# Optimization experiments

Measured on AMD Instinct MI355X. Metric: run time of the kernel, lower is better.

## Reference

```python
import jax, jax.numpy as jnp
import numpy as np
from jax import lax

N_RAYS, N_STEPS, G = 4096, 160, 160
COLOR_DIM, WIDTH = 3, 128
POS_PE, VIEW_PE = 5, 4
XYZ_MIN, XYZ_MAX = -1.0, 1.0
NEAR = 0.05
STEPSIZE = 0.5
VOXEL_SIZE = (XYZ_MAX - XYZ_MIN) / G
DIST = STEPSIZE * VOXEL_SIZE
S_VAL = 80.0
FASTCOLOR_THRES = 1e-7
MASK_THRES = 1e-3
ALPHA_INIT = 1e-4
ACT_SHIFT = float(np.log(1.0 / (1.0 - ALPHA_INIT) - 1.0))
SMOOTH_K, SMOOTH_SIGMA = 5, 1.0
POSFREQ = jnp.asarray([2.0 ** i for i in range(POS_PE)], jnp.float32)
VIEWFREQ = jnp.asarray([2.0 ** i for i in range(VIEW_PE)], jnp.float32)


def _gauss_kernel():
    ax = np.arange(SMOOTH_K) - SMOOTH_K // 2
    g = np.exp(-(ax ** 2) / (2.0 * SMOOTH_SIGMA ** 2))
    k = g[:, None, None] * g[None, :, None] * g[None, None, :]
    return jnp.asarray(k / k.sum(), np.float32)[None, None]


def _trilerp(grid, pts):
    # grid [C,Gx,Gx,Gx]; pts [...,3] in world coords -> [..., C] (align_corners trilinear)
    Gx = grid.shape[-1]
    u = (pts - XYZ_MIN) / (XYZ_MAX - XYZ_MIN) * (Gx - 1)
    u = jnp.clip(u, 0.0, Gx - 1.0)
    i0 = jnp.clip(jnp.floor(u).astype(jnp.int32), 0, Gx - 2)
    f = u - i0.astype(u.dtype)
    x0, y0, z0 = i0[..., 0], i0[..., 1], i0[..., 2]
    fx, fy, fz = f[..., 0], f[..., 1], f[..., 2]
    def g8(ix, iy, iz):
        return grid[:, ix, iy, iz]  # [C, ...]
    out = (g8(x0, y0, z0) * (1 - fx) * (1 - fy) * (1 - fz)
         + g8(x0, y0, z0 + 1) * (1 - fx) * (1 - fy) * fz
         + g8(x0, y0 + 1, z0) * (1 - fx) * fy * (1 - fz)
         + g8(x0, y0 + 1, z0 + 1) * (1 - fx) * fy * fz
         + g8(x0 + 1, y0, z0) * fx * (1 - fy) * (1 - fz)
         + g8(x0 + 1, y0, z0 + 1) * fx * (1 - fy) * fz
         + g8(x0 + 1, y0 + 1, z0) * fx * fy * (1 - fz)
         + g8(x0 + 1, y0 + 1, z0 + 1) * fx * fy * fz)
    return jnp.moveaxis(out, 0, -1)


def _alphas2weights(alpha):
    # per-ray (segmented) exclusive cumprod of transmittance; alpha [N,S]
    T = jnp.cumprod(1.0 - alpha, axis=1)
    T_excl = jnp.concatenate([jnp.ones_like(T[:, :1]), T[:, :-1]], axis=1)
    return alpha * T_excl, T[:, -1]


def _mlp(x, w0, b0, w1, b1, w2, b2):
    h = jax.nn.relu(x @ w0 + b0)
    h = jax.nn.relu(h @ w1 + b1)
    return h @ w2 + b2


def _forward(rays_o, rays_d, viewdirs, sdf_grid, mask_density,
             off_color_grid, emo_color_grid,
             off_w0, off_b0, off_w1, off_b1, off_w2, off_b2,
             emo_w0, emo_b0, emo_w1, emo_b1, emo_w2, emo_b2, em_modes):
    N = rays_o.shape[0]
    t = NEAR + DIST * jnp.arange(N_STEPS, dtype=jnp.float32)
    ray_pts = rays_o[:, None, :] + rays_d[:, None, :] * t[None, :, None]  # [N,S,3]

    # MaskCache: threshold alpha from coarse density grid (boolean keep mask)
    dens = _trilerp(mask_density, ray_pts)[..., 0]
    mask_alpha = 1.0 - jnp.exp(-jax.nn.softplus(dens + ACT_SHIFT) * DIST)
    keep0 = mask_alpha >= MASK_THRES  # [N,S]

    # Gaussian-smoothed SDF grid + central-difference gradient grid
    sdf_s = lax.conv_general_dilated(sdf_grid, _gauss_kernel(), (1, 1, 1), 'SAME',
                                     dimension_numbers=('NCDHW', 'OIDHW', 'NCDHW'))[0]  # [1,G,G,G]
    s = sdf_s[0]
    grad_grid = jnp.zeros((3, G, G, G), sdf_grid.dtype)
    grad_grid = grad_grid.at[0, 1:-1].set((s[2:] - s[:-2]) / (2 * VOXEL_SIZE))
    grad_grid = grad_grid.at[1, :, 1:-1].set((s[:, 2:] - s[:, :-2]) / (2 * VOXEL_SIZE))
    grad_grid = grad_grid.at[2, :, :, 1:-1].set((s[:, :, 2:] - s[:, :, :-2]) / (2 * VOXEL_SIZE))

    sdf = _trilerp(sdf_s, ray_pts)[..., 0]   # [N,S]
    gradient = _trilerp(grad_grid, ray_pts)  # [N,S,3]

    # NeuS alpha from sdf (scatter, grad variant, cos_anneal = 1)
    true_cos = jnp.einsum('nd,nsd->ns', viewdirs, gradient)
    iter_cos = -jax.nn.relu(-true_cos)
    prev_cdf = jax.nn.sigmoid((sdf - iter_cos * DIST * 0.5) * S_VAL)
    next_cdf = jax.nn.sigmoid((sdf + iter_cos * DIST * 0.5) * S_VAL)
    alpha = jnp.clip((prev_cdf - next_cdf + 1e-5) / (prev_cdf + 1e-5), 0.0, 1.0)
    alpha = jnp.where(keep0, alpha, 0.0)  # masked points contribute nothing

    weights, _ = _alphas2weights(alpha)
    keep1 = weights > FASTCOLOR_THRES
    alpha = jnp.where(keep1, alpha, 0.0)
    weights, alphainv_last = _alphas2weights(alpha)

    # features: pos PE, view PE (per-ray, gathered by ray_id == broadcast), normal
    rays_xyz = (ray_pts - XYZ_MIN) / (XYZ_MAX - XYZ_MIN)  # [N,S,3]
    xyz_emb = (rays_xyz[..., None] * POSFREQ).reshape(N, N_STEPS, -1)
    v_emb = (viewdirs[..., None] * VIEWFREQ).reshape(N, -1)
    v_full = jnp.concatenate([v_emb, jnp.sin(v_emb), jnp.cos(v_emb)], -1)
    v_full = jnp.broadcast_to(v_full[:, None, :], (N, N_STEPS, v_full.shape[-1]))
    normal = gradient / (jnp.linalg.norm(gradient, axis=-1, keepdims=True) + 1e-5)
    rgb_feat = jnp.concatenate([rays_xyz, jnp.sin(xyz_emb), jnp.cos(xyz_emb), v_full, normal], -1)

    off_in = jnp.concatenate([_trilerp(off_color_grid, ray_pts), rgb_feat], -1)
    emo_in = jnp.concatenate([_trilerp(emo_color_grid, ray_pts), rgb_feat], -1)
    off_rgb = jax.nn.sigmoid(_mlp(off_in, off_w0, off_b0, off_w1, off_b1, off_w2, off_b2))
    emo_rgb = jax.nn.sigmoid(_mlp(emo_in, emo_w0, emo_b0, emo_w1, emo_b1, emo_w2, emo_b2))
    on_mask = (em_modes == 1)[:, None, None]  # em_modes[ray_id] == 1
    rgb = jnp.where(on_mask, emo_rgb, 0.0) + off_rgb

    w_ = weights[..., None]
    rgb_marched = jnp.sum(w_ * rgb, axis=1)  # segment_coo(sum over ray_id)
    cum_weights = jnp.sum(w_, axis=1)        # [N,1]
    return rgb_marched, alphainv_last, 1.0 - cum_weights


def setup_inputs() -> dict:
    key = jax.random.key(0)
    ks = jax.random.split(key, 12)
    rays_o = jax.random.uniform(ks[0], (N_RAYS, 3), jnp.float32, -0.3, 0.3)
    rd = jax.random.normal(ks[1], (N_RAYS, 3), jnp.float32)
    rays_d = rd / jnp.linalg.norm(rd, axis=-1, keepdims=True)
    viewdirs = rays_d
    em_modes = jax.random.randint(ks[2], (N_RAYS,), 0, 2)
    lin = np.linspace(-1.0, 1.0, G, dtype=np.float32)
    x, y, z = np.meshgrid(lin, lin, lin, indexing='ij')
    sdf_grid = jnp.asarray(np.sqrt(x ** 2 + y ** 2 + z ** 2) - 1.0)[None, None]  # sphere-SDF init
    mask_density = jax.random.normal(ks[3], (1, 80, 80, 80), jnp.float32) * 2.0 + 12.0
    off_color_grid = jax.random.normal(ks[4], (COLOR_DIM, G, G, G), jnp.float32) * 0.1
    emo_color_grid = jax.random.normal(ks[5], (COLOR_DIM, G, G, G), jnp.float32) * 0.1
    DIM0 = 3 + 3 * POS_PE * 2 + 3 * VIEW_PE * 3 + COLOR_DIM + 3  # = 75
    def lw(k, i, o):
        return jax.random.normal(k, (i, o), jnp.float32) * (1.0 / np.sqrt(i))
    return dict(rays_o=rays_o, rays_d=rays_d, viewdirs=viewdirs, em_modes=em_modes,
                sdf_grid=sdf_grid, mask_density=mask_density,
                off_color_grid=off_color_grid, emo_color_grid=emo_color_grid,
                off_w0=lw(ks[6], DIM0, WIDTH), off_b0=jnp.zeros((WIDTH,), jnp.float32),
                off_w1=lw(ks[7], WIDTH, WIDTH), off_b1=jnp.zeros((WIDTH,), jnp.float32),
                off_w2=lw(ks[8], WIDTH, 3), off_b2=jnp.zeros((3,), jnp.float32),
                emo_w0=lw(ks[9], DIM0, WIDTH), emo_b0=jnp.zeros((WIDTH,), jnp.float32),
                emo_w1=lw(ks[10], WIDTH, WIDTH), emo_b1=jnp.zeros((WIDTH,), jnp.float32),
                emo_w2=lw(ks[11], WIDTH, 3), emo_b2=jnp.zeros((3,), jnp.float32))


def reference(rays_o, rays_d, viewdirs, em_modes, sdf_grid, mask_density,
              off_color_grid, emo_color_grid,
              off_w0, off_b0, off_w1, off_b1, off_w2, off_b2,
              emo_w0, emo_b0, emo_w1, emo_b1, emo_w2, emo_b2):
    return _forward(rays_o, rays_d, viewdirs, sdf_grid, mask_density,
                    off_color_grid, emo_color_grid,
                    off_w0, off_b0, off_w1, off_b1, off_w2, off_b2,
                    emo_w0, emo_b0, emo_w1, emo_b1, emo_w2, emo_b2, em_modes)
```

## Files before the change

kernel.cpp:

```cpp
#include <hip/hip_runtime.h>

#define NRAYS 4096
#define NSTEPS 160
#define NSAMP (NRAYS*NSTEPS)
#define GG 160
#define GG2 (GG*GG)
#define GG3 (GG*GG2)
#define GM 80
#define GM2 (GM*GM)

#define NEARV 0.05f
#define DISTV 0.00625f
#define SVAL 80.0f
#define ACT_SHIFT_C (-9.2102403669758813f)
#define INV2H 40.0f
#define MASK_THRES_C 1e-3f
#define FAST_THRES_C 1e-7f

#define KW0 0.05448868454964295f
#define KW1 0.24420134200323332f
#define KW2 0.40261994689424750f

__device__ __forceinline__ float sigmf(float x){ return 1.0f/(1.0f+__expf(-x)); }
__device__ __forceinline__ float softplusf_(float x){ return (x>20.0f)? x : log1pf(__expf(x)); }

__device__ __forceinline__ void tricoord(float p, int Gx, int& i0, float& fr){
  float u = (p + 1.0f)*0.5f*(float)(Gx-1);
  u = fminf(fmaxf(u, 0.0f), (float)(Gx-1));
  int i = (int)floorf(u);
  i = min(max(i,0), Gx-2);
  i0 = i; fr = u - (float)i;
}

__global__ __launch_bounds__(256) void ksmooth_yz(const float* __restrict__ in, float* __restrict__ out,
                                                  float* __restrict__ outbuf, int* __restrict__ cnt){
  __shared__ float S[36][37];
  __shared__ float Tz[36][33];
  const int bx = blockIdx.x;
  const int t = threadIdx.x;
  if (bx == 0){
    for (int i = t; i < NRAYS*3; i += 256) outbuf[i] = 0.0f;
    if (t == 0) *cnt = 0;
  }
  const int x  = bx / 25;
  const int tile = bx % 25;
  const int Y0 = (tile/5)*32, Z0 = (tile%5)*32;
  const float kw[5] = {KW0,KW1,KW2,KW1,KW0};
  for (int i = t; i < 36*36; i += 256){
    int r = i/36, c = i - (i/36)*36;
    int y = Y0 + r - 2, z = Z0 + c - 2;
    float v = 0.0f;
    if (y>=0 && y<GG && z>=0 && z<GG) v = in[(x*GG+y)*GG+z];
    S[r][c] = v;
  }
  __syncthreads();
  for (int i = t; i < 36*32; i += 256){
    int r = i >> 5, c = i & 31;
    float acc = 0.f;
    #pragma unroll
    for (int d=0; d<5; d++) acc += kw[d]*S[r][c+d];
    Tz[r][c] = acc;
  }
  __syncthreads();
  for (int i = t; i < 32*32; i += 256){
    int yy = i >> 5, c = i & 31;
    float acc = 0.f;
    #pragma unroll
    for (int d=0; d<5; d++) acc += kw[d]*Tz[yy+d][c];
    out[(x*GG + Y0+yy)*GG + Z0 + c] = acc;
  }
}

__global__ __launch_bounds__(64) void kmarch(
  const float* __restrict__ ro, const float* __restrict__ rd,
  const float* __restrict__ vd, const float* __restrict__ maskg,
  const float* __restrict__ Y,
  int* __restrict__ slist, float* __restrict__ sw, float* __restrict__ sgrad,
  int* __restrict__ cnt, float* __restrict__ out)
{
  int n = blockIdx.x*64 + threadIdx.x;
  if (n >= NRAYS) return;
  const float ox=ro[n*3+0], oy=ro[n*3+1], oz=ro[n*3+2];
  const float dx=rd[n*3+0], dy=rd[n*3+1], dz=rd[n*3+2];
  const float vx=vd[n*3+0], vy=vd[n*3+1], vz=vd[n*3+2];
  const float kwc[5] = {KW0,KW1,KW2,KW1,KW0};
  float T1=1.0f, T2=1.0f, cum=0.0f;
  for (int s=0; s<NSTEPS; s++){
    float tt = NEARV + DISTV*(float)s;
    float px = ox + dx*tt, py = oy + dy*tt, pz = oz + dz*tt;

    int mx,my,mz; float mfx,mfy,mfz;
    tricoord(px, GM, mx, mfx); tricoord(py, GM, my, mfy); tricoord(pz, GM, mz, mfz);
    int mid = (mx*GM + my)*GM + mz;
    float d000=maskg[mid],        d001=maskg[mid+1];
    float d010=maskg[mid+GM],     d011=maskg[mid+GM+1];
    float d100=maskg[mid+GM2],    d101=maskg[mid+GM2+1];
    float d110=maskg[mid+GM2+GM], d111=maskg[mid+GM2+GM+1];
    float m00 = d000 + (d001-d000)*mfz;
    float m01 = d010 + (d011-d010)*mfz;
    float m10 = d100 + (d101-d100)*mfz;
    float m11 = d110 + (d111-d110)*mfz;
    float m0 = m00 + (m01-m00)*mfy;
    float m1 = m10 + (m11-m10)*mfy;
    float dens = m0 + (m1-m0)*mfx;
    float malpha = 1.0f - __expf(-softplusf_(dens + ACT_SHIFT_C)*DISTV);

    int ix,iy,iz; float fx,fy,fz;
    tricoord(px, GG, ix, fx); tricoord(py, GG, iy, fy); tricoord(pz, GG, iz, fz);

    float R[2][2][8];
    #pragma unroll
    for (int jb=0;jb<2;jb++)
      #pragma unroll
      for (int jc=0;jc<2;jc++)
        #pragma unroll
        for (int j=0;j<8;j++){
          int a = ix-3+j;
          R[jb][jc][j] = (a>=0 && a<GG) ? Y[(a*GG + iy+jb)*GG + iz+jc] : 0.0f;
        }
    const bool hasym = (iy>=1), hasyp = (iy<=GG-3);
    const bool haszm = (iz>=1), haszp = (iz<=GG-3);
    float Eym[2][6], Eyp[2][6], Ezm[2][6], Ezp[2][6];
    #pragma unroll
    for (int jc=0;jc<2;jc++)
      #pragma unroll
      for (int j=0;j<6;j++){
        int a = ix-2+j;
        bool ax = (a>=0 && a<GG);
        Eym[jc][j] = (hasym && ax) ? Y[(a*GG + iy-1)*GG + iz+jc] : 0.0f;
        Eyp[jc][j] = (hasyp && ax) ? Y[(a*GG + iy+2)*GG + iz+jc] : 0.0f;
      }
    #pragma unroll
    for (int jb=0;jb<2;jb++)
      #pragma unroll
      for (int j=0;j<6;j++){
        int a = ix-2+j;
        bool ax = (a>=0 && a<GG);
        Ezm[jb][j] = (haszm && ax) ? Y[(a*GG + iy+jb)*GG + iz-1] : 0.0f;
        Ezp[jb][j] = (haszp && ax) ? Y[(a*GG + iy+jb)*GG + iz+2] : 0.0f;
      }

    float sdf=0.0f, gx=0.0f, gy=0.0f, gz=0.0f;
    #pragma unroll
    for (int ja=0;ja<2;ja++){
      #pragma unroll
      for (int jb=0;jb<2;jb++){
        #pragma unroll
        for (int jc=0;jc<2;jc++){
          float w = (ja?fx:1.0f-fx)*(jb?fy:1.0f-fy)*(jc?fz:1.0f-fz);
          const float* r = R[jb][jc];
          float s0=0.0f;
          #pragma unroll
          for (int t2=0;t2<5;t2++) s0 += kwc[t2]*r[ja+1+t2];
          sdf += w*s0;
          int a = ix+ja, b = iy+jb, c = iz+jc;
          if (a>=1 && a<=GG-2){
            float sp=0.0f, sm=0.0f;
            #pragma unroll
            for (int t2=0;t2<5;t2++){ sp += kwc[t2]*r[ja+2+t2]; sm += kwc[t2]*r[ja+t2]; }
            gx += w*INV2H*(sp-sm);
          }
          if (b>=1 && b<=GG-2){
            float acc=0.0f;
            if (jb==0){
              const float* up = R[1][jc];
              const float* dn = Eym[jc];
              #pragma unroll
              for (int t2=0;t2<5;t2++) acc += kwc[t2]*(up[ja+1+t2] - dn[ja+t2]);
            } else {
              const float* up = Eyp[jc];
              const float* dn = R[0][jc];
              #pragma unroll
              for (int t2=0;t2<5;t2++) acc += kwc[t2]*(up[ja+t2] - dn[ja+1+t2]);
            }
            gy += w*INV2H*acc;
          }
          if (c>=1 && c<=GG-2){
            float acc=0.0f;
            if (jc==0){
              const float* up = R[jb][1];
              const float* dn = Ezm[jb];
              #pragma unroll
              for (int t2=0;t2<5;t2++) acc += kwc[t2]*(up[ja+1+t2] - dn[ja+t2]);
            } else {
              const float* up = Ezp[jb];
              const float* dn = R[jb][0];
              #pragma unroll
              for (int t2=0;t2<5;t2++) acc += kwc[t2]*(up[ja+t2] - dn[ja+1+t2]);
            }
            gz += w*INV2H*acc;
          }
        }
      }
    }

    float tc = vx*gx + vy*gy + vz*gz;
    float icos = fminf(tc, 0.0f);
    float e = icos*DISTV*0.5f;
    float prev = sigmf((sdf - e)*SVAL);
    float nxt  = sigmf((sdf + e)*SVAL);
    float alpha = (prev - nxt + 1e-5f)/(prev + 1e-5f);
    alpha = fminf(fmaxf(alpha, 0.0f), 1.0f);
    if (!(malpha >= MASK_THRES_C)) alpha = 0.0f;

    float w1 = alpha*T1; T1 *= (1.0f - alpha);
    float a2 = (w1 > FAST_THRES_C) ? alpha : 0.0f;
    float wv = a2*T2;   T2 *= (1.0f - a2);
    cum += wv;
    if (wv > 0.0f){
      int pos = atomicAdd(cnt, 1);
      slist[pos] = n*NSTEPS + s;
      sw[pos] = wv;
      sgrad[pos*3+0]=gx; sgrad[pos*3+1]=gy; sgrad[pos*3+2]=gz;
    }
    if (T1 <= FAST_THRES_C) break;
  }
  out[NRAYS*3 + n] = T2;
  out[NRAYS*4 + n] = 1.0f - cum;
}

__global__ __launch_bounds__(256) void kmlp3(
  const float* __restrict__ ro, const float* __restrict__ rd,
  const float* __restrict__ vd, const int* __restrict__ em,
  const float* __restrict__ offc, const float* __restrict__ emoc,
  const int* __restrict__ slist, const float* __restrict__ sw,
  const float* __restrict__ sgrad, const int* __restrict__ cnt,
  const float* __restrict__ W0o, const float* __restrict__ b0o,
  const float* __restrict__ W1o, const float* __restrict__ b1o,
  const float* __restrict__ W2o, const float* __restrict__ b2o,
  const float* __restrict__ W0e, const float* __restrict__ b0e,
  const float* __restrict__ W1e, const float* __restrict__ b1e,
  const float* __restrict__ W2e, const float* __restrict__ b2e,
  float* __restrict__ out)
{
  __shared__ float X[8][80];
  __shared__ float H[8][132];
  __shared__ float H2[8][132];
  __shared__ float OUTB[8][3];
  __shared__ float WSH[8];
  __shared__ float GS[8][3];
  __shared__ int SSAMP[8];
  __shared__ int SEM[8];
  __shared__ int s_go;

  const int t = threadIdx.x;
  const int count = *cnt;
  const int head = blockIdx.x & 1;
  const int cstride = gridDim.x >> 1;

  const float* W0 = head ? W0e : W0o;  const float* b0 = head ? b0e : b0o;
  const float* W1 = head ? W1e : W1o;  const float* b1 = head ? b1e : b1o;
  const float* W2 = head ? W2e : W2o;  const float* b2 = head ? b2e : b2o;
  const float* cg = head ? emoc : offc;
  const float4* W04 = (const float4*)W0;
  const float4* W14 = (const float4*)W1;

  const int sp   = t >> 5;
  const int lane = t & 31;

  for (int chunk = blockIdx.x >> 1; chunk*8 < count; chunk += cstride) {
    const int base = chunk*8;
    if (t == 0) s_go = 0;
    if (t < 8) {
      int i = base + t;
      bool vld = (i < count);
      int samp = vld ? slist[i] : 0;
      SSAMP[t] = samp;
      WSH[t]   = vld ? sw[i] : 0.0f;
      GS[t][0] = vld ? sgrad[i*3+0] : 0.0f;
      GS[t][1] = vld ? sgrad[i*3+1] : 0.0f;
      GS[t][2] = vld ? sgrad[i*3+2] : 0.0f;
      SEM[t]   = vld ? em[samp/NSTEPS] : 0;
    }
    __syncthreads();
    if (t < 8) {
      bool live = (WSH[t] > 0.0f) && (head == 0 || SEM[t] != 0);
      if (live) s_go = 1;
    }
    __syncthreads();

    if (s_go) {
      {
        const int s = t & 7;
        const int r = t >> 3;
        const int samp = SSAMP[s];
        const int n = samp / NSTEPS;
        const int step = samp - n*NSTEPS;
        const float tt = NEARV + DISTV*(float)step;
        const float px = ro[n*3+0] + rd[n*3+0]*tt;
        const float py = ro[n*3+1] + rd[n*3+1]*tt;
        const float pz = ro[n*3+2] + rd[n*3+2]*tt;
        if (r < 3) {
          int ix,iy,iz; float fx,fy,fz;
          tricoord(px, GG, ix, fx); tricoord(py, GG, iy, fy); tricoord(pz, GG, iz, fz);
          const float* g = cg + (size_t)r * GG3;
          const int id = (ix*GG + iy)*GG + iz;
          float v000=g[id],        v001=g[id+1];
          float v010=g[id+GG],     v011=g[id+GG+1];
          float v100=g[id+GG2],    v101=g[id+GG2+1];
          float v110=g[id+GG2+GG], v111=g[id+GG2+GG+1];
          float c00 = v000 + (v001-v000)*fz;
          float c01 = v010 + (v011-v010)*fz;
          float c10 = v100 + (v101-v100)*fz;
          float c11 = v110 + (v111-v110)*fz;
          float c0 = c00 + (c01-c00)*fy;
          float c1 = c10 + (c11-c10)*fy;
          X[s][r] = c0 + (c1-c0)*fx;
        } else if (r == 3) {
          X[s][3] = (px+1.0f)*0.5f;
          X[s][4] = (py+1.0f)*0.5f;
          X[s][5] = (pz+1.0f)*0.5f;
          float gx = GS[s][0], gy = GS[s][1], gz = GS[s][2];
          float inv = 1.0f/(sqrtf(gx*gx+gy*gy+gz*gz)+1e-5f);
          X[s][72] = gx*inv; X[s][73] = gy*inv; X[s][74] = gz*inv;
        } else if (r < 7) {
          const int a = r - 4;
          const float coord = (a==0)?px:((a==1)?py:pz);
          const float rxyz = (coord+1.0f)*0.5f;
          float fr = 1.0f;
          #pragma unroll
          for (int q = 0; q < 5; q++) {
            float e = rxyz*fr; fr *= 2.0f;
            X[s][6  + a*5 + q] = __sinf(e);
            X[s][21 + a*5 + q] = __cosf(e);
          }
        } else if (r < 10) {
          const int a = r - 7;
          const float v = vd[n*3+a];
          float fr = 1.0f;
          #pragma unroll
          for (int q = 0; q < 4; q++) {
            float e = v*fr; fr *= 2.0f;
            X[s][36 + a*4 + q] = e;
            X[s][48 + a*4 + q] = __sinf(e);
            X[s][60 + a*4 + q] = __cosf(e);
          }
        }
      }
      __syncthreads();

      {
        float4 acc = ((const float4*)b0)[lane];
        #pragma unroll 5
        for (int k=0; k<75; k++){
          float x = X[sp][k];
          float4 w = W04[k*32 + lane];
          acc.x += x*w.x; acc.y += x*w.y; acc.z += x*w.z; acc.w += x*w.w;
        }
        H[sp][lane*4+0] = fmaxf(acc.x,0.0f);
        H[sp][lane*4+1] = fmaxf(acc.y,0.0f);
        H[sp][lane*4+2] = fmaxf(acc.z,0.0f);
        H[sp][lane*4+3] = fmaxf(acc.w,0.0f);
      }
      __syncthreads();

      {
        float4 acc = ((const float4*)b1)[lane];
        #pragma unroll 8
        for (int k=0; k<128; k++){
          float x = H[sp][k];
          float4 w = W14[k*32 + lane];
          acc.x += x*w.x; acc.y += x*w.y; acc.z += x*w.z; acc.w += x*w.w;
        }
        H2[sp][lane*4+0] = fmaxf(acc.x,0.0f);
        H2[sp][lane*4+1] = fmaxf(acc.y,0.0f);
        H2[sp][lane*4+2] = fmaxf(acc.z,0.0f);
        H2[sp][lane*4+3] = fmaxf(acc.w,0.0f);
      }
      __syncthreads();

      {
        float a0=0.0f, a1=0.0f, a2v=0.0f;
        #pragma unroll
        for (int i=0;i<4;i++){
          int k = lane*4+i;
          float h = H2[sp][k];
          a0  += h*W2[k*3+0];
          a1  += h*W2[k*3+1];
          a2v += h*W2[k*3+2];
        }
        #pragma unroll
        for (int d=16; d>=1; d>>=1){
          a0  += __shfl_down(a0,  d, 32);
          a1  += __shfl_down(a1,  d, 32);
          a2v += __shfl_down(a2v, d, 32);
        }
        if (lane == 0){
          OUTB[sp][0] = sigmf(a0  + b2[0]);
          OUTB[sp][1] = sigmf(a1  + b2[1]);
          OUTB[sp][2] = sigmf(a2v + b2[2]);
        }
      }
      __syncthreads();

      if (t < 24) {
        int s2 = t/3, c = t - s2*3;
        float w = WSH[s2];
        if (w > 0.0f && (head == 0 || SEM[s2] != 0)) {
          int n2 = SSAMP[s2]/NSTEPS;
          atomicAdd(&out[n2*3 + c], w * OUTB[s2][c]);
        }
      }
    }
    __syncthreads();
  }
}

extern "C" void kernel_launch(void* const* d_in, const int* in_sizes, int n_in,
                              void* d_out, int out_size, void* d_ws, size_t ws_size,
                              hipStream_t stream) {
  const float* ro    = (const float*)d_in[0];
  const float* rd    = (const float*)d_in[1];
  const float* vd    = (const float*)d_in[2];
  const int*   em    = (const int*)d_in[3];
  const float* sdfg  = (const float*)d_in[4];
  const float* maskg = (const float*)d_in[5];
  const float* offc  = (const float*)d_in[6];
  const float* emoc  = (const float*)d_in[7];
  const float* W0o = (const float*)d_in[8];
  const float* b0o = (const float*)d_in[9];
  const float* W1o = (const float*)d_in[10];
  const float* b1o = (const float*)d_in[11];
  const float* W2o = (const float*)d_in[12];
  const float* b2o = (const float*)d_in[13];
  const float* W0e = (const float*)d_in[14];
  const float* b0e = (const float*)d_in[15];
  const float* W1e = (const float*)d_in[16];
  const float* b1e = (const float*)d_in[17];
  const float* W2e = (const float*)d_in[18];
  const float* b2e = (const float*)d_in[19];

  float* out = (float*)d_out;
  float* ws  = (float*)d_ws;
  float* bufB  = ws;
  float* swb   = ws + GG3;
  float* sgradb= swb + NSAMP;
  int*   slist = (int*)(sgradb + 3*(size_t)NSAMP);
  int*   cnt   = slist + NSAMP;

  ksmooth_yz<<<GG*25, 256, 0, stream>>>(sdfg, bufB, out, cnt);

  kmarch<<<NRAYS/64, 64, 0, stream>>>(ro, rd, vd, maskg, bufB,
                                      slist, swb, sgradb, cnt, out);

  kmlp3<<<2048, 256, 0, stream>>>(ro, rd, vd, em, offc, emoc,
                                  slist, swb, sgradb, cnt,
                                  W0o,b0o,W1o,b1o,W2o,b2o,
                                  W0e,b0e,W1e,b1e,W2e,b2e, out);
}
```

Baseline: 66.89 us.

## Fuse smoothing, ray march and MLP into one cooperative kernel

```diff
diff --git a/kernel.cpp b/kernel.cpp
--- a/kernel.cpp
+++ b/kernel.cpp
@@ -1,4 +1,6 @@
 #include <hip/hip_runtime.h>
+#include <hip/hip_cooperative_groups.h>
+namespace cg = cooperative_groups;
 
 #define NRAYS 4096
 #define NSTEPS 160
@@ -32,207 +34,22 @@
   i0 = i; fr = u - (float)i;
 }
 
-__global__ __launch_bounds__(256) void ksmooth_yz(const float* __restrict__ in, float* __restrict__ out,
-                                                  float* __restrict__ outbuf, int* __restrict__ cnt){
-  __shared__ float S[36][37];
-  __shared__ float Tz[36][33];
-  const int bx = blockIdx.x;
-  const int t = threadIdx.x;
-  if (bx == 0){
-    for (int i = t; i < NRAYS*3; i += 256) outbuf[i] = 0.0f;
-    if (t == 0) *cnt = 0;
-  }
-  const int x  = bx / 25;
-  const int tile = bx % 25;
-  const int Y0 = (tile/5)*32, Z0 = (tile%5)*32;
-  const float kw[5] = {KW0,KW1,KW2,KW1,KW0};
-  for (int i = t; i < 36*36; i += 256){
-    int r = i/36, c = i - (i/36)*36;
-    int y = Y0 + r - 2, z = Z0 + c - 2;
-    float v = 0.0f;
-    if (y>=0 && y<GG && z>=0 && z<GG) v = in[(x*GG+y)*GG+z];
-    S[r][c] = v;
-  }
-  __syncthreads();
-  for (int i = t; i < 36*32; i += 256){
-    int r = i >> 5, c = i & 31;
-    float acc = 0.f;
-    #pragma unroll
-    for (int d=0; d<5; d++) acc += kw[d]*S[r][c+d];
-    Tz[r][c] = acc;
-  }
-  __syncthreads();
-  for (int i = t; i < 32*32; i += 256){
-    int yy = i >> 5, c = i & 31;
-    float acc = 0.f;
-    #pragma unroll
-    for (int d=0; d<5; d++) acc += kw[d]*Tz[yy+d][c];
-    out[(x*GG + Y0+yy)*GG + Z0 + c] = acc;
-  }
-}
-
-__global__ __launch_bounds__(64) void kmarch(
-  const float* __restrict__ ro, const float* __restrict__ rd,
-  const float* __restrict__ vd, const float* __restrict__ maskg,
-  const float* __restrict__ Y,
-  int* __restrict__ slist, float* __restrict__ sw, float* __restrict__ sgrad,
-  int* __restrict__ cnt, float* __restrict__ out)
-{
-  int n = blockIdx.x*64 + threadIdx.x;
-  if (n >= NRAYS) return;
-  const float ox=ro[n*3+0], oy=ro[n*3+1], oz=ro[n*3+2];
-  const float dx=rd[n*3+0], dy=rd[n*3+1], dz=rd[n*3+2];
-  const float vx=vd[n*3+0], vy=vd[n*3+1], vz=vd[n*3+2];
-  const float kwc[5] = {KW0,KW1,KW2,KW1,KW0};
-  float T1=1.0f, T2=1.0f, cum=0.0f;
-  for (int s=0; s<NSTEPS; s++){
-    float tt = NEARV + DISTV*(float)s;
-    float px = ox + dx*tt, py = oy + dy*tt, pz = oz + dz*tt;
-
-    int mx,my,mz; float mfx,mfy,mfz;
-    tricoord(px, GM, mx, mfx); tricoord(py, GM, my, mfy); tricoord(pz, GM, mz, mfz);
-    int mid = (mx*GM + my)*GM + mz;
-    float d000=maskg[mid],        d001=maskg[mid+1];
-    float d010=maskg[mid+GM],     d011=maskg[mid+GM+1];
-    float d100=maskg[mid+GM2],    d101=maskg[mid+GM2+1];
-    float d110=maskg[mid+GM2+GM], d111=maskg[mid+GM2+GM+1];
-    float m00 = d000 + (d001-d000)*mfz;
-    float m01 = d010 + (d011-d010)*mfz;
-    float m10 = d100 + (d101-d100)*mfz;
-    float m11 = d110 + (d111-d110)*mfz;
-    float m0 = m00 + (m01-m00)*mfy;
-    float m1 = m10 + (m11-m10)*mfy;
-    float dens = m0 + (m1-m0)*mfx;
-    float malpha = 1.0f - __expf(-softplusf_(dens + ACT_SHIFT_C)*DISTV);
-
-    int ix,iy,iz; float fx,fy,fz;
-    tricoord(px, GG, ix, fx); tricoord(py, GG, iy, fy); tricoord(pz, GG, iz, fz);
-
-    float R[2][2][8];
-    #pragma unroll
-    for (int jb=0;jb<2;jb++)
-      #pragma unroll
-      for (int jc=0;jc<2;jc++)
-        #pragma unroll
-        for (int j=0;j<8;j++){
-          int a = ix-3+j;
-          R[jb][jc][j] = (a>=0 && a<GG) ? Y[(a*GG + iy+jb)*GG + iz+jc] : 0.0f;
-        }
-    const bool hasym = (iy>=1), hasyp = (iy<=GG-3);
-    const bool haszm = (iz>=1), haszp = (iz<=GG-3);
-    float Eym[2][6], Eyp[2][6], Ezm[2][6], Ezp[2][6];
-    #pragma unroll
-    for (int jc=0;jc<2;jc++)
-      #pragma unroll
-      for (int j=0;j<6;j++){
-        int a = ix-2+j;
-        bool ax = (a>=0 && a<GG);
-        Eym[jc][j] = (hasym && ax) ? Y[(a*GG + iy-1)*GG + iz+jc] : 0.0f;
-        Eyp[jc][j] = (hasyp && ax) ? Y[(a*GG + iy+2)*GG + iz+jc] : 0.0f;
-      }
-    #pragma unroll
-    for (int jb=0;jb<2;jb++)
-      #pragma unroll
-      for (int j=0;j<6;j++){
-        int a = ix-2+j;
-        bool ax = (a>=0 && a<GG);
-        Ezm[jb][j] = (haszm && ax) ? Y[(a*GG + iy+jb)*GG + iz-1] : 0.0f;
-        Ezp[jb][j] = (haszp && ax) ? Y[(a*GG + iy+jb)*GG + iz+2] : 0.0f;
-      }
-
-    float sdf=0.0f, gx=0.0f, gy=0.0f, gz=0.0f;
-    #pragma unroll
-    for (int ja=0;ja<2;ja++){
-      #pragma unroll
-      for (int jb=0;jb<2;jb++){
-        #pragma unroll
-        for (int jc=0;jc<2;jc++){
-          float w = (ja?fx:1.0f-fx)*(jb?fy:1.0f-fy)*(jc?fz:1.0f-fz);
-          const float* r = R[jb][jc];
-          float s0=0.0f;
-          #pragma unroll
-          for (int t2=0;t2<5;t2++) s0 += kwc[t2]*r[ja+1+t2];
-          sdf += w*s0;
-          int a = ix+ja, b = iy+jb, c = iz+jc;
-          if (a>=1 && a<=GG-2){
-            float sp=0.0f, sm=0.0f;
-            #pragma unroll
-            for (int t2=0;t2<5;t2++){ sp += kwc[t2]*r[ja+2+t2]; sm += kwc[t2]*r[ja+t2]; }
-            gx += w*INV2H*(sp-sm);
-          }
-          if (b>=1 && b<=GG-2){
-            float acc=0.0f;
-            if (jb==0){
-              const float* up = R[1][jc];
-              const float* dn = Eym[jc];
-              #pragma unroll
-              for (int t2=0;t2<5;t2++) acc += kwc[t2]*(up[ja+1+t2] - dn[ja+t2]);
-            } else {
-              const float* up = Eyp[jc];
-              const float* dn = R[0][jc];
-              #pragma unroll
-              for (int t2=0;t2<5;t2++) acc += kwc[t2]*(up[ja+t2] - dn[ja+1+t2]);
-            }
-            gy += w*INV2H*acc;
-          }
-          if (c>=1 && c<=GG-2){
-            float acc=0.0f;
-            if (jc==0){
-              const float* up = R[jb][1];
-              const float* dn = Ezm[jb];
-              #pragma unroll
-              for (int t2=0;t2<5;t2++) acc += kwc[t2]*(up[ja+1+t2] - dn[ja+t2]);
-            } else {
-              const float* up = Ezp[jb];
-              const float* dn = R[jb][0];
-              #pragma unroll
-              for (int t2=0;t2<5;t2++) acc += kwc[t2]*(up[ja+t2] - dn[ja+1+t2]);
-            }
-            gz += w*INV2H*acc;
-          }
-        }
-      }
-    }
-
-    float tc = vx*gx + vy*gy + vz*gz;
-    float icos = fminf(tc, 0.0f);
-    float e = icos*DISTV*0.5f;
-    float prev = sigmf((sdf - e)*SVAL);
-    float nxt  = sigmf((sdf + e)*SVAL);
-    float alpha = (prev - nxt + 1e-5f)/(prev + 1e-5f);
-    alpha = fminf(fmaxf(alpha, 0.0f), 1.0f);
-    if (!(malpha >= MASK_THRES_C)) alpha = 0.0f;
-
-    float w1 = alpha*T1; T1 *= (1.0f - alpha);
-    float a2 = (w1 > FAST_THRES_C) ? alpha : 0.0f;
-    float wv = a2*T2;   T2 *= (1.0f - a2);
-    cum += wv;
-    if (wv > 0.0f){
-      int pos = atomicAdd(cnt, 1);
-      slist[pos] = n*NSTEPS + s;
-      sw[pos] = wv;
-      sgrad[pos*3+0]=gx; sgrad[pos*3+1]=gy; sgrad[pos*3+2]=gz;
-    }
-    if (T1 <= FAST_THRES_C) break;
-  }
-  out[NRAYS*3 + n] = T2;
-  out[NRAYS*4 + n] = 1.0f - cum;
-}
-
-__global__ __launch_bounds__(256) void kmlp3(
+__global__ __launch_bounds__(256) void kfused(
   const float* __restrict__ ro, const float* __restrict__ rd,
   const float* __restrict__ vd, const int* __restrict__ em,
+  const float* __restrict__ sdfg, const float* __restrict__ maskg,
   const float* __restrict__ offc, const float* __restrict__ emoc,
-  const int* __restrict__ slist, const float* __restrict__ sw,
-  const float* __restrict__ sgrad, const int* __restrict__ cnt,
   const float* __restrict__ W0o, const float* __restrict__ b0o,
   const float* __restrict__ W1o, const float* __restrict__ b1o,
   const float* __restrict__ W2o, const float* __restrict__ b2o,
   const float* __restrict__ W0e, const float* __restrict__ b0e,
   const float* __restrict__ W1e, const float* __restrict__ b1e,
   const float* __restrict__ W2e, const float* __restrict__ b2e,
-  float* __restrict__ out)
+  float* __restrict__ Y, int* __restrict__ slist, float* __restrict__ sw,
+  float* __restrict__ sgrad, int* __restrict__ cnt, float* __restrict__ out)
 {
+  __shared__ float S[36][37];
+  __shared__ float Tz[36][33];
   __shared__ float X[8][80];
   __shared__ float H[8][132];
   __shared__ float H2[8][132];
@@ -243,166 +60,356 @@
   __shared__ int SEM[8];
   __shared__ int s_go;
 
+  const int bid = blockIdx.x;
   const int t = threadIdx.x;
-  const int count = *cnt;
-  const int head = blockIdx.x & 1;
-  const int cstride = gridDim.x >> 1;
-
-  const float* W0 = head ? W0e : W0o;  const float* b0 = head ? b0e : b0o;
-  const float* W1 = head ? W1e : W1o;  const float* b1 = head ? b1e : b1o;
-  const float* W2 = head ? W2e : W2o;  const float* b2 = head ? b2e : b2o;
-  const float* cg = head ? emoc : offc;
-  const float4* W04 = (const float4*)W0;
-  const float4* W14 = (const float4*)W1;
-
-  const int sp   = t >> 5;
-  const int lane = t & 31;
-
-  for (int chunk = blockIdx.x >> 1; chunk*8 < count; chunk += cstride) {
-    const int base = chunk*8;
-    if (t == 0) s_go = 0;
-    if (t < 8) {
-      int i = base + t;
-      bool vld = (i < count);
-      int samp = vld ? slist[i] : 0;
-      SSAMP[t] = samp;
-      WSH[t]   = vld ? sw[i] : 0.0f;
-      GS[t][0] = vld ? sgrad[i*3+0] : 0.0f;
-      GS[t][1] = vld ? sgrad[i*3+1] : 0.0f;
-      GS[t][2] = vld ? sgrad[i*3+2] : 0.0f;
-      SEM[t]   = vld ? em[samp/NSTEPS] : 0;
+  cg::grid_group grid = cg::this_grid();
+
+  if (bid == 0){
+    for (int i = t; i < NRAYS*3; i += 256) out[i] = 0.0f;
+    if (t == 0) *cnt = 0;
+  }
+
+  {
+    const float kw[5] = {KW0,KW1,KW2,KW1,KW0};
+    for (int tl = bid; tl < GG*25; tl += gridDim.x){
+      __syncthreads();
+      const int x  = tl / 25;
+      const int tile = tl % 25;
+      const int Y0 = (tile/5)*32, Z0 = (tile%5)*32;
+      for (int i = t; i < 36*36; i += 256){
+        int r = i/36, c = i - (i/36)*36;
+        int y = Y0 + r - 2, z = Z0 + c - 2;
+        float v = 0.0f;
+        if (y>=0 && y<GG && z>=0 && z<GG) v = sdfg[(x*GG+y)*GG+z];
+        S[r][c] = v;
+      }
+      __syncthreads();
+      for (int i = t; i < 36*32; i += 256){
+        int r = i >> 5, c = i & 31;
+        float acc = 0.f;
+        #pragma unroll
+        for (int d=0; d<5; d++) acc += kw[d]*S[r][c+d];
+        Tz[r][c] = acc;
+      }
+      __syncthreads();
+      for (int i = t; i < 32*32; i += 256){
+        int yy = i >> 5, c = i & 31;
+        float acc = 0.f;
+        #pragma unroll
+        for (int d=0; d<5; d++) acc += kw[d]*Tz[yy+d][c];
+        Y[(x*GG + Y0+yy)*GG + Z0 + c] = acc;
+      }
     }
-    __syncthreads();
-    if (t < 8) {
-      bool live = (WSH[t] > 0.0f) && (head == 0 || SEM[t] != 0);
-      if (live) s_go = 1;
+  }
+  __threadfence();
+  grid.sync();
+
+  {
+    const int n = bid*256 + t;
+    if (n < NRAYS){
+      const float ox=ro[n*3+0], oy=ro[n*3+1], oz=ro[n*3+2];
+      const float dx=rd[n*3+0], dy=rd[n*3+1], dz=rd[n*3+2];
+      const float vx=vd[n*3+0], vy=vd[n*3+1], vz=vd[n*3+2];
+      const float kwc[5] = {KW0,KW1,KW2,KW1,KW0};
+      float T1=1.0f, T2=1.0f, cum=0.0f;
+      for (int s=0; s<NSTEPS; s++){
+        float tt = NEARV + DISTV*(float)s;
+        float px = ox + dx*tt, py = oy + dy*tt, pz = oz + dz*tt;
+
+        int mx,my,mz; float mfx,mfy,mfz;
+        tricoord(px, GM, mx, mfx); tricoord(py, GM, my, mfy); tricoord(pz, GM, mz, mfz);
+        int mid = (mx*GM + my)*GM + mz;
+        float d000=maskg[mid],        d001=maskg[mid+1];
+        float d010=maskg[mid+GM],     d011=maskg[mid+GM+1];
+        float d100=maskg[mid+GM2],    d101=maskg[mid+GM2+1];
+        float d110=maskg[mid+GM2+GM], d111=maskg[mid+GM2+GM+1];
+        float m00 = d000 + (d001-d000)*mfz;
+        float m01 = d010 + (d011-d010)*mfz;
+        float m10 = d100 + (d101-d100)*mfz;
+        float m11 = d110 + (d111-d110)*mfz;
+        float m0 = m00 + (m01-m00)*mfy;
+        float m1 = m10 + (m11-m10)*mfy;
+        float dens = m0 + (m1-m0)*mfx;
+        float malpha = 1.0f - __expf(-softplusf_(dens + ACT_SHIFT_C)*DISTV);
+
+        int ix,iy,iz; float fx,fy,fz;
+        tricoord(px, GG, ix, fx); tricoord(py, GG, iy, fy); tricoord(pz, GG, iz, fz);
+
+        float R[2][2][8];
+        #pragma unroll
+        for (int jb=0;jb<2;jb++)
+          #pragma unroll
+          for (int jc=0;jc<2;jc++)
+            #pragma unroll
+            for (int j=0;j<8;j++){
+              int a = ix-3+j;
+              R[jb][jc][j] = (a>=0 && a<GG) ? Y[(a*GG + iy+jb)*GG + iz+jc] : 0.0f;
+            }
+        const bool hasym = (iy>=1), hasyp = (iy<=GG-3);
+        const bool haszm = (iz>=1), haszp = (iz<=GG-3);
+        float Eym[2][6], Eyp[2][6], Ezm[2][6], Ezp[2][6];
+        #pragma unroll
+        for (int jc=0;jc<2;jc++)
+          #pragma unroll
+          for (int j=0;j<6;j++){
+            int a = ix-2+j;
+            bool ax = (a>=0 && a<GG);
+            Eym[jc][j] = (hasym && ax) ? Y[(a*GG + iy-1)*GG + iz+jc] : 0.0f;
+            Eyp[jc][j] = (hasyp && ax) ? Y[(a*GG + iy+2)*GG + iz+jc] : 0.0f;
+          }
+        #pragma unroll
+        for (int jb=0;jb<2;jb++)
+          #pragma unroll
+          for (int j=0;j<6;j++){
+            int a = ix-2+j;
+            bool ax = (a>=0 && a<GG);
+            Ezm[jb][j] = (haszm && ax) ? Y[(a*GG + iy+jb)*GG + iz-1] : 0.0f;
+            Ezp[jb][j] = (haszp && ax) ? Y[(a*GG + iy+jb)*GG + iz+2] : 0.0f;
+          }
+
+        float sdf=0.0f, gx=0.0f, gy=0.0f, gz=0.0f;
+        #pragma unroll
+        for (int ja=0;ja<2;ja++){
+          #pragma unroll
+          for (int jb=0;jb<2;jb++){
+            #pragma unroll
+            for (int jc=0;jc<2;jc++){
+              float w = (ja?fx:1.0f-fx)*(jb?fy:1.0f-fy)*(jc?fz:1.0f-fz);
+              const float* r = R[jb][jc];
+              float s0=0.0f;
+              #pragma unroll
+              for (int t2=0;t2<5;t2++) s0 += kwc[t2]*r[ja+1+t2];
+              sdf += w*s0;
+              int a = ix+ja, b = iy+jb, c = iz+jc;
+              if (a>=1 && a<=GG-2){
+                float sp=0.0f, sm=0.0f;
+                #pragma unroll
+                for (int t2=0;t2<5;t2++){ sp += kwc[t2]*r[ja+2+t2]; sm += kwc[t2]*r[ja+t2]; }
+                gx += w*INV2H*(sp-sm);
+              }
+              if (b>=1 && b<=GG-2){
+                float acc=0.0f;
+                if (jb==0){
+                  const float* up = R[1][jc];
+                  const float* dn = Eym[jc];
+                  #pragma unroll
+                  for (int t2=0;t2<5;t2++) acc += kwc[t2]*(up[ja+1+t2] - dn[ja+t2]);
+                } else {
+                  const float* up = Eyp[jc];
+                  const float* dn = R[0][jc];
+                  #pragma unroll
+                  for (int t2=0;t2<5;t2++) acc += kwc[t2]*(up[ja+t2] - dn[ja+1+t2]);
+                }
+                gy += w*INV2H*acc;
+              }
+              if (c>=1 && c<=GG-2){
+                float acc=0.0f;
+                if (jc==0){
+                  const float* up = R[jb][1];
+                  const float* dn = Ezm[jb];
+                  #pragma unroll
+                  for (int t2=0;t2<5;t2++) acc += kwc[t2]*(up[ja+1+t2] - dn[ja+t2]);
+                } else {
+                  const float* up = Ezp[jb];
+                  const float* dn = R[jb][0];
+                  #pragma unroll
+                  for (int t2=0;t2<5;t2++) acc += kwc[t2]*(up[ja+t2] - dn[ja+1+t2]);
+                }
+                gz += w*INV2H*acc;
+              }
+            }
+          }
+        }
+
+        float tc = vx*gx + vy*gy + vz*gz;
+        float icos = fminf(tc, 0.0f);
+        float e = icos*DISTV*0.5f;
+        float prev = sigmf((sdf - e)*SVAL);
+        float nxt  = sigmf((sdf + e)*SVAL);
+        float alpha = (prev - nxt + 1e-5f)/(prev + 1e-5f);
+        alpha = fminf(fmaxf(alpha, 0.0f), 1.0f);
+        if (!(malpha >= MASK_THRES_C)) alpha = 0.0f;
+
+        float w1 = alpha*T1; T1 *= (1.0f - alpha);
+        float a2 = (w1 > FAST_THRES_C) ? alpha : 0.0f;
+        float wv = a2*T2;   T2 *= (1.0f - a2);
+        cum += wv;
+        if (wv > 0.0f){
+          int pos = atomicAdd(cnt, 1);
+          slist[pos] = n*NSTEPS + s;
+          sw[pos] = wv;
+          sgrad[pos*3+0]=gx; sgrad[pos*3+1]=gy; sgrad[pos*3+2]=gz;
+        }
+        if (T1 <= FAST_THRES_C) break;
+      }
+      out[NRAYS*3 + n] = T2;
+      out[NRAYS*4 + n] = 1.0f - cum;
     }
-    __syncthreads();
-
-    if (s_go) {
-      {
-        const int s = t & 7;
-        const int r = t >> 3;
-        const int samp = SSAMP[s];
-        const int n = samp / NSTEPS;
-        const int step = samp - n*NSTEPS;
-        const float tt = NEARV + DISTV*(float)step;
-        const float px = ro[n*3+0] + rd[n*3+0]*tt;
-        const float py = ro[n*3+1] + rd[n*3+1]*tt;
-        const float pz = ro[n*3+2] + rd[n*3+2]*tt;
-        if (r < 3) {
-          int ix,iy,iz; float fx,fy,fz;
-          tricoord(px, GG, ix, fx); tricoord(py, GG, iy, fy); tricoord(pz, GG, iz, fz);
-          const float* g = cg + (size_t)r * GG3;
-          const int id = (ix*GG + iy)*GG + iz;
-          float v000=g[id],        v001=g[id+1];
-          float v010=g[id+GG],     v011=g[id+GG+1];
-          float v100=g[id+GG2],    v101=g[id+GG2+1];
-          float v110=g[id+GG2+GG], v111=g[id+GG2+GG+1];
-          float c00 = v000 + (v001-v000)*fz;
-          float c01 = v010 + (v011-v010)*fz;
-          float c10 = v100 + (v101-v100)*fz;
-          float c11 = v110 + (v111-v110)*fz;
-          float c0 = c00 + (c01-c00)*fy;
-          float c1 = c10 + (c11-c10)*fy;
-          X[s][r] = c0 + (c1-c0)*fx;
-        } else if (r == 3) {
-          X[s][3] = (px+1.0f)*0.5f;
-          X[s][4] = (py+1.0f)*0.5f;
-          X[s][5] = (pz+1.0f)*0.5f;
-          float gx = GS[s][0], gy = GS[s][1], gz = GS[s][2];
-          float inv = 1.0f/(sqrtf(gx*gx+gy*gy+gz*gz)+1e-5f);
-          X[s][72] = gx*inv; X[s][73] = gy*inv; X[s][74] = gz*inv;
-        } else if (r < 7) {
-          const int a = r - 4;
-          const float coord = (a==0)?px:((a==1)?py:pz);
-          const float rxyz = (coord+1.0f)*0.5f;
-          float fr = 1.0f;
-          #pragma unroll
-          for (int q = 0; q < 5; q++) {
-            float e = rxyz*fr; fr *= 2.0f;
-            X[s][6  + a*5 + q] = __sinf(e);
-            X[s][21 + a*5 + q] = __cosf(e);
-          }
-        } else if (r < 10) {
-          const int a = r - 7;
-          const float v = vd[n*3+a];
-          float fr = 1.0f;
-          #pragma unroll
-          for (int q = 0; q < 4; q++) {
-            float e = v*fr; fr *= 2.0f;
-            X[s][36 + a*4 + q] = e;
-            X[s][48 + a*4 + q] = __sinf(e);
-            X[s][60 + a*4 + q] = __cosf(e);
-          }
-        }
-      }
-      __syncthreads();
-
-      {
-        float4 acc = ((const float4*)b0)[lane];
-        #pragma unroll 5
-        for (int k=0; k<75; k++){
-          float x = X[sp][k];
-          float4 w = W04[k*32 + lane];
-          acc.x += x*w.x; acc.y += x*w.y; acc.z += x*w.z; acc.w += x*w.w;
-        }
-        H[sp][lane*4+0] = fmaxf(acc.x,0.0f);
-        H[sp][lane*4+1] = fmaxf(acc.y,0.0f);
-        H[sp][lane*4+2] = fmaxf(acc.z,0.0f);
-        H[sp][lane*4+3] = fmaxf(acc.w,0.0f);
-      }
-      __syncthreads();
-
-      {
-        float4 acc = ((const float4*)b1)[lane];
-        #pragma unroll 8
-        for (int k=0; k<128; k++){
-          float x = H[sp][k];
-          float4 w = W14[k*32 + lane];
-          acc.x += x*w.x; acc.y += x*w.y; acc.z += x*w.z; acc.w += x*w.w;
-        }
-        H2[sp][lane*4+0] = fmaxf(acc.x,0.0f);
-        H2[sp][lane*4+1] = fmaxf(acc.y,0.0f);
-        H2[sp][lane*4+2] = fmaxf(acc.z,0.0f);
-        H2[sp][lane*4+3] = fmaxf(acc.w,0.0f);
-      }
-      __syncthreads();
-
-      {
-        float a0=0.0f, a1=0.0f, a2v=0.0f;
-        #pragma unroll
-        for (int i=0;i<4;i++){
-          int k = lane*4+i;
-          float h = H2[sp][k];
-          a0  += h*W2[k*3+0];
-          a1  += h*W2[k*3+1];
-          a2v += h*W2[k*3+2];
-        }
-        #pragma unroll
-        for (int d=16; d>=1; d>>=1){
-          a0  += __shfl_down(a0,  d, 32);
-          a1  += __shfl_down(a1,  d, 32);
-          a2v += __shfl_down(a2v, d, 32);
-        }
-        if (lane == 0){
-          OUTB[sp][0] = sigmf(a0  + b2[0]);
-          OUTB[sp][1] = sigmf(a1  + b2[1]);
-          OUTB[sp][2] = sigmf(a2v + b2[2]);
-        }
-      }
-      __syncthreads();
-
-      if (t < 24) {
-        int s2 = t/3, c = t - s2*3;
-        float w = WSH[s2];
-        if (w > 0.0f && (head == 0 || SEM[s2] != 0)) {
-          int n2 = SSAMP[s2]/NSTEPS;
-          atomicAdd(&out[n2*3 + c], w * OUTB[s2][c]);
-        }
-      }
+  }
+  __threadfence();
+  grid.sync();
+
+  {
+    const int count = *cnt;
+    const int head = bid & 1;
+    const int cstride = gridDim.x >> 1;
+
+    const float* W0 = head ? W0e : W0o;  const float* b0 = head ? b0e : b0o;
+    const float* W1 = head ? W1e : W1o;  const float* b1 = head ? b1e : b1o;
+    const float* W2 = head ? W2e : W2o;  const float* b2 = head ? b2e : b2o;
+    const float* cg2 = head ? emoc : offc;
+    const float4* W04 = (const float4*)W0;
+    const float4* W14 = (const float4*)W1;
+
+    const int sp   = t >> 5;
+    const int lane = t & 31;
+
+    for (int chunk = bid >> 1; chunk*8 < count; chunk += cstride) {
+      const int base = chunk*8;
+      if (t == 0) s_go = 0;
+      if (t < 8) {
+        int i = base + t;
+        bool vld = (i < count);
+        int samp = vld ? slist[i] : 0;
+        SSAMP[t] = samp;
+        WSH[t]   = vld ? sw[i] : 0.0f;
+        GS[t][0] = vld ? sgrad[i*3+0] : 0.0f;
+        GS[t][1] = vld ? sgrad[i*3+1] : 0.0f;
+        GS[t][2] = vld ? sgrad[i*3+2] : 0.0f;
+        SEM[t]   = vld ? em[samp/NSTEPS] : 0;
+      }
+      __syncthreads();
+      if (t < 8) {
+        bool live = (WSH[t] > 0.0f) && (head == 0 || SEM[t] != 0);
+        if (live) s_go = 1;
+      }
+      __syncthreads();
+
+      if (s_go) {
+        {
+          const int s = t & 7;
+          const int r = t >> 3;
+          const int samp = SSAMP[s];
+          const int n = samp / NSTEPS;
+          const int step = samp - n*NSTEPS;
+          const float tt = NEARV + DISTV*(float)step;
+          const float px = ro[n*3+0] + rd[n*3+0]*tt;
+          const float py = ro[n*3+1] + rd[n*3+1]*tt;
+          const float pz = ro[n*3+2] + rd[n*3+2]*tt;
+          if (r < 3) {
+            int ix,iy,iz; float fx,fy,fz;
+            tricoord(px, GG, ix, fx); tricoord(py, GG, iy, fy); tricoord(pz, GG, iz, fz);
+            const float* g = cg2 + (size_t)r * GG3;
+            const int id = (ix*GG + iy)*GG + iz;
+            float v000=g[id],        v001=g[id+1];
+            float v010=g[id+GG],     v011=g[id+GG+1];
+            float v100=g[id+GG2],    v101=g[id+GG2+1];
+            float v110=g[id+GG2+GG], v111=g[id+GG2+GG+1];
+            float c00 = v000 + (v001-v000)*fz;
+            float c01 = v010 + (v011-v010)*fz;
+            float c10 = v100 + (v101-v100)*fz;
+            float c11 = v110 + (v111-v110)*fz;
+            float c0 = c00 + (c01-c00)*fy;
+            float c1 = c10 + (c11-c10)*fy;
+            X[s][r] = c0 + (c1-c0)*fx;
+          } else if (r == 3) {
+            X[s][3] = (px+1.0f)*0.5f;
+            X[s][4] = (py+1.0f)*0.5f;
+            X[s][5] = (pz+1.0f)*0.5f;
+            float gx = GS[s][0], gy = GS[s][1], gz = GS[s][2];
+            float inv = 1.0f/(sqrtf(gx*gx+gy*gy+gz*gz)+1e-5f);
+            X[s][72] = gx*inv; X[s][73] = gy*inv; X[s][74] = gz*inv;
+          } else if (r < 7) {
+            const int a = r - 4;
+            const float coord = (a==0)?px:((a==1)?py:pz);
+            const float rxyz = (coord+1.0f)*0.5f;
+            float fr = 1.0f;
+            #pragma unroll
+            for (int q = 0; q < 5; q++) {
+              float e = rxyz*fr; fr *= 2.0f;
+              X[s][6  + a*5 + q] = __sinf(e);
+              X[s][21 + a*5 + q] = __cosf(e);
+            }
+          } else if (r < 10) {
+            const int a = r - 7;
+            const float v = vd[n*3+a];
+            float fr = 1.0f;
+            #pragma unroll
+            for (int q = 0; q < 4; q++) {
+              float e = v*fr; fr *= 2.0f;
+              X[s][36 + a*4 + q] = e;
+              X[s][48 + a*4 + q] = __sinf(e);
+              X[s][60 + a*4 + q] = __cosf(e);
+            }
+          }
+        }
+        __syncthreads();
+
+        {
+          float4 acc = ((const float4*)b0)[lane];
+          #pragma unroll 5
+          for (int k=0; k<75; k++){
+            float x = X[sp][k];
+            float4 w = W04[k*32 + lane];
+            acc.x += x*w.x; acc.y += x*w.y; acc.z += x*w.z; acc.w += x*w.w;
+          }
+          H[sp][lane*4+0] = fmaxf(acc.x,0.0f);
+          H[sp][lane*4+1] = fmaxf(acc.y,0.0f);
+          H[sp][lane*4+2] = fmaxf(acc.z,0.0f);
+          H[sp][lane*4+3] = fmaxf(acc.w,0.0f);
+        }
+        __syncthreads();
+
+        {
+          float4 acc = ((const float4*)b1)[lane];
+          #pragma unroll 8
+          for (int k=0; k<128; k++){
+            float x = H[sp][k];
+            float4 w = W14[k*32 + lane];
+            acc.x += x*w.x; acc.y += x*w.y; acc.z += x*w.z; acc.w += x*w.w;
+          }
+          H2[sp][lane*4+0] = fmaxf(acc.x,0.0f);
+          H2[sp][lane*4+1] = fmaxf(acc.y,0.0f);
+          H2[sp][lane*4+2] = fmaxf(acc.z,0.0f);
+          H2[sp][lane*4+3] = fmaxf(acc.w,0.0f);
+        }
+        __syncthreads();
+
+        {
+          float a0=0.0f, a1=0.0f, a2v=0.0f;
+          #pragma unroll
+          for (int i=0;i<4;i++){
+            int k = lane*4+i;
+            float h = H2[sp][k];
+            a0  += h*W2[k*3+0];
+            a1  += h*W2[k*3+1];
+            a2v += h*W2[k*3+2];
+          }
+          #pragma unroll
+          for (int d=16; d>=1; d>>=1){
+            a0  += __shfl_down(a0,  d, 32);
+            a1  += __shfl_down(a1,  d, 32);
+            a2v += __shfl_down(a2v, d, 32);
+          }
+          if (lane == 0){
+            OUTB[sp][0] = sigmf(a0  + b2[0]);
+            OUTB[sp][1] = sigmf(a1  + b2[1]);
+            OUTB[sp][2] = sigmf(a2v + b2[2]);
+          }
+        }
+        __syncthreads();
+
+        if (t < 24) {
+          int s2 = t/3, c = t - s2*3;
+          float w = WSH[s2];
+          if (w > 0.0f && (head == 0 || SEM[s2] != 0)) {
+            int n2 = SSAMP[s2]/NSTEPS;
+            atomicAdd(&out[n2*3 + c], w * OUTB[s2][c]);
+          }
+        }
+      }
+      __syncthreads();
     }
-    __syncthreads();
   }
 }
 
@@ -432,19 +439,18 @@
 
   float* out = (float*)d_out;
   float* ws  = (float*)d_ws;
-  float* bufB  = ws;
+  float* Yb    = ws;
   float* swb   = ws + GG3;
   float* sgradb= swb + NSAMP;
   int*   slist = (int*)(sgradb + 3*(size_t)NSAMP);
   int*   cnt   = slist + NSAMP;
 
-  ksmooth_yz<<<GG*25, 256, 0, stream>>>(sdfg, bufB, out, cnt);
-
-  kmarch<<<NRAYS/64, 64, 0, stream>>>(ro, rd, vd, maskg, bufB,
-                                      slist, swb, sgradb, cnt, out);
-
-  kmlp3<<<2048, 256, 0, stream>>>(ro, rd, vd, em, offc, emoc,
-                                  slist, swb, sgradb, cnt,
-                                  W0o,b0o,W1o,b1o,W2o,b2o,
-                                  W0e,b0e,W1e,b1e,W2e,b2e, out);
+  void* args[] = {
+    &ro,&rd,&vd,&em,&sdfg,&maskg,&offc,&emoc,
+    &W0o,&b0o,&W1o,&b1o,&W2o,&b2o,
+    &W0e,&b0e,&W1e,&b1e,&W2e,&b2e,
+    &Yb,&slist,&swb,&sgradb,&cnt,&out
+  };
+  hipLaunchCooperativeKernel((const void*)kfused, dim3(256), dim3(256),
+                             args, 0, stream);
 }
```

New measurement: 239.9 us. 3.59x slower.
